# Optimization experiments

Measured on AMD Instinct MI355X. Metric: run time of the kernel, lower is better.

Reference implementation:

```python
import jax, jax.numpy as jnp
import numpy as np

N_NODES = 40000
N_EDGES = 640000
D = 128
N_LAYERS = 3


def setup_inputs() -> dict:
    key = jax.random.key(0)
    ks = jax.random.split(key, 6)
    x = jax.random.normal(ks[0], (N_NODES, D), dtype=jnp.float32)
    src = jax.random.randint(ks[1], (N_EDGES,), 0, N_NODES, dtype=jnp.int32)
    dst = jax.random.randint(ks[2], (N_EDGES,), 0, N_NODES, dtype=jnp.int32)
    scale = 1.0 / np.sqrt(D)
    w_self = jax.random.normal(ks[3], (N_LAYERS, D, D), dtype=jnp.float32) * scale
    w_neigh = jax.random.normal(ks[4], (N_LAYERS, D, D), dtype=jnp.float32) * scale
    b = jax.random.normal(ks[5], (N_LAYERS, D), dtype=jnp.float32) * scale
    return {"x": x, "src": src, "dst": dst, "w_self": w_self, "w_neigh": w_neigh, "b": b}


def reference(x, src, dst, w_self, w_neigh, b):
    # in-degree per destination node (clamped to avoid div-by-zero, matching mean aggregator)
    deg = jax.ops.segment_sum(jnp.ones_like(dst, dtype=x.dtype), dst, num_segments=N_NODES)
    inv_deg = (1.0 / jnp.maximum(deg, 1.0))[:, None]  # [N,1]

    h = x
    for l in range(N_LAYERS):
        # mean aggregation over in-neighbors: gather src feats, scatter-add to dst
        agg = jax.ops.segment_sum(h[src], dst, num_segments=N_NODES) * inv_deg  # [N,D]
        h = h @ w_self[l] + agg @ w_neigh[l] + b[l]  # SAGEConv: fc_self + fc_neigh + bias
        if l < N_LAYERS - 1:
            h = jax.nn.relu(h)  # dropout p=0.0 -> identity
    return h
```

## Files before the change

kernel.cpp:

```cpp
#include <hip/hip_runtime.h>

#define N_NODES 40000
#define N_EDGES 640000
#define DIM 128
#define N_LAYERS 3
#define STRIDE 64

typedef _Float16 half_t;
typedef __attribute__((ext_vector_type(8))) _Float16 f16x8_t;
typedef __attribute__((ext_vector_type(4))) float f32x4_t;

__global__ void scatterprep_kernel(const int* __restrict__ src, const int* __restrict__ dst,
                                   int* __restrict__ cnt, unsigned short* __restrict__ pcsr,
                                   const float* __restrict__ x, half_t* __restrict__ h,
                                   unsigned char* __restrict__ hq, float* __restrict__ hsc,
                                   const float* __restrict__ w_self, const float* __restrict__ w_neigh,
                                   half_t* __restrict__ wt) {
    const int SB = (N_EDGES + 255) / 256;
    if (blockIdx.x < SB) {
        int i = blockIdx.x * 256 + threadIdx.x;
        if (i < N_EDGES) {
            int d = dst[i];
            int pos = atomicAdd(&cnt[d], 1);
            if (pos < STRIDE) pcsr[d * STRIDE + pos] = (unsigned short)src[i];
        }
        return;
    }
    int i = (blockIdx.x - SB) * 256 + threadIdx.x;
    const int NS = N_NODES * DIM / 8;
    if (i < NS) {
        const float4* p = (const float4*)x + (size_t)i * 2;
        float4 a = p[0], b2 = p[1];
        float v[8] = {a.x, a.y, a.z, a.w, b2.x, b2.y, b2.z, b2.w};
        f16x8_t hv;
        float mx = 0.f;
#pragma unroll
        for (int j = 0; j < 8; ++j) {
            hv[j] = (half_t)v[j];
            mx = fmaxf(mx, fabsf((float)hv[j]));
        }
        *(f16x8_t*)&h[(size_t)i * 8] = hv;
        mx = fmaxf(mx, __shfl_xor(mx, 1));
        mx = fmaxf(mx, __shfl_xor(mx, 2));
        mx = fmaxf(mx, __shfl_xor(mx, 4));
        mx = fmaxf(mx, __shfl_xor(mx, 8));
        mx = fmaxf(mx, 1e-20f);
        float inv = 127.f / mx;
        unsigned int lo = 0, hi = 0;
#pragma unroll
        for (int j = 0; j < 4; ++j) {
            int q = (int)rintf((float)hv[j] * inv) + 128;
            lo |= ((unsigned int)q) << (8 * j);
        }
#pragma unroll
        for (int j = 0; j < 4; ++j) {
            int q = (int)rintf((float)hv[4 + j] * inv) + 128;
            hi |= ((unsigned int)q) << (8 * j);
        }
        uint2 pk; pk.x = lo; pk.y = hi;
        *(uint2*)&hq[(size_t)i * 8] = pk;
        if ((i & 15) == 0) hsc[i >> 4] = mx / 127.f;
    } else {
        int j = i - NS;
        if (j < N_LAYERS * 2 * DIM * DIM) {
            int k = j & (DIM - 1);
            int n = (j >> 7) & (DIM - 1);
            int ls = j >> 14;
            int l = ls >> 1, s = ls & 1;
            const float* W = (s ? w_neigh : w_self) + (size_t)l * DIM * DIM;
            wt[j] = (half_t)W[k * DIM + n];
        }
    }
}

__global__ void agg_kernel(const unsigned char* __restrict__ hq, const float* __restrict__ hsc,
                           const int* __restrict__ cnt, const unsigned short* __restrict__ pcsr,
                           half_t* __restrict__ agg) {
    int node = (blockIdx.x * blockDim.x + threadIdx.x) >> 6;
    int lane = threadIdx.x & 63;
    if (node >= N_NODES) return;
    const int g = lane >> 4, c = lane & 15;
    int deg = cnt[node];
    int nd = deg < STRIDE ? deg : STRIDE;
    int il = (lane < nd) ? (int)pcsr[node * STRIDE + lane] : 0;
    float sl = (lane < nd) ? hsc[il] : 0.f;

    float acc[8] = {0.f, 0.f, 0.f, 0.f, 0.f, 0.f, 0.f, 0.f};
    float ssum = 0.f;
    for (int base = 0; base < nd; base += 16) {
        float sf[4];
        int sidx[4];
        uint2 q[4];
#pragma unroll
        for (int s = 0; s < 4; ++s) {
            int ee = base + 4 * s + g;
            sidx[s] = __shfl(il, ee, 64);
            sf[s] = __shfl(sl, ee, 64);
            q[s] = *(const uint2*)&hq[(size_t)sidx[s] * DIM + c * 8];
        }
#pragma unroll
        for (int s = 0; s < 4; ++s) {
            ssum += sf[s];
            unsigned int lo = q[s].x, hi = q[s].y;
#pragma unroll
            for (int j = 0; j < 4; ++j)
                acc[j] = fmaf(sf[s], (float)((lo >> (8 * j)) & 0xFF), acc[j]);
#pragma unroll
            for (int j = 0; j < 4; ++j)
                acc[4 + j] = fmaf(sf[s], (float)((hi >> (8 * j)) & 0xFF), acc[4 + j]);
        }
    }
#pragma unroll
    for (int j = 0; j < 8; ++j) acc[j] -= 128.f * ssum;
#pragma unroll
    for (int j = 0; j < 8; ++j) {
        acc[j] += __shfl_xor(acc[j], 16, 64);
        acc[j] += __shfl_xor(acc[j], 32, 64);
    }
    if (g == 0) {
        float w = 1.0f / fmaxf((float)deg, 1.0f);
        f16x8_t o;
#pragma unroll
        for (int j = 0; j < 8; ++j) o[j] = (half_t)(acc[j] * w);
        *(f16x8_t*)&agg[(size_t)node * DIM + c * 8] = o;
    }
}

#define LDSN 136
#define SCRP 132
__global__ __launch_bounds__(256) void gemm_kernel(
    half_t* __restrict__ h, const half_t* __restrict__ agg,
    const half_t* __restrict__ wt,
    const float* __restrict__ bias, float* __restrict__ fout,
    unsigned char* __restrict__ hq, float* __restrict__ hsc,
    int write_f32, int relu) {
    __shared__ half_t sW[2 * DIM][LDSN];
    half_t (*sScr)[SCRP] = (half_t(*)[SCRP])sW;
    const int tid = threadIdx.x;
    const int wave = tid >> 6, lane = tid & 63;
    const int quad = lane >> 4, m = lane & 15;
    const int rowW = blockIdx.x * 128 + wave * 32;

#pragma unroll
    for (int c4 = 0; c4 < 16; ++c4) {
        int c = (c4 << 8) + tid;
        int part = c & 15;
        int n = c >> 4;
        *(f16x8_t*)&sW[n][part * 8] = *(const f16x8_t*)&wt[(size_t)n * DIM + part * 8];
    }
    __syncthreads();

    f32x4_t acc[2][8];
#pragma unroll
    for (int a = 0; a < 2; ++a)
#pragma unroll
        for (int b = 0; b < 8; ++b) acc[a][b] = {0.f, 0.f, 0.f, 0.f};

#pragma unroll
    for (int s = 0; s < 2; ++s) {
        const half_t* A = s ? agg : h;
        const int nb = s * DIM;
#pragma unroll
        for (int k2 = 0; k2 < 4; ++k2) {
            const int kg = (k2 << 5) + quad * 8;
            f16x8_t B[8];
#pragma unroll
            for (int jt = 0; jt < 8; ++jt)
                B[jt] = *(const f16x8_t*)&sW[nb + jt * 16 + m][kg];
#pragma unroll
            for (int rt = 0; rt < 2; ++rt) {
                int r = rowW + rt * 16 + m;
                r = (r < N_NODES) ? r : (N_NODES - 1);
                f16x8_t a = *(const f16x8_t*)&A[(size_t)r * DIM + kg];
#pragma unroll
                for (int jt = 0; jt < 8; ++jt)
                    acc[rt][jt] = __builtin_amdgcn_mfma_f32_16x16x32_f16(a, B[jt], acc[rt][jt], 0, 0, 0);
            }
        }
    }

    __syncthreads();

#pragma unroll
    for (int rt = 0; rt < 2; ++rt)
#pragma unroll
        for (int jt = 0; jt < 8; ++jt) {
            int col = jt * 16 + m;
            float bv = bias[col];
#pragma unroll
            for (int r4 = 0; r4 < 4; ++r4) {
                int rloc = wave * 32 + rt * 16 + quad * 4 + r4;
                int row = blockIdx.x * 128 + rloc;
                if (row >= N_NODES) continue;
                float v = acc[rt][jt][r4] + bv;
                if (relu) v = fmaxf(v, 0.f);
                if (write_f32) {
                    fout[(size_t)row * DIM + col] = v;
                } else {
                    half_t hv = (half_t)v;
                    h[(size_t)row * DIM + col] = hv;
                    sScr[rloc][col] = hv;
                }
            }
        }

    if (!write_f32) {
        __syncthreads();
        int rl = tid >> 1, hf = tid & 1;
        int row = blockIdx.x * 128 + rl;
        if (row < N_NODES) {
            float mx = 0.f;
#pragma unroll
            for (int k8 = 0; k8 < 8; ++k8) {
                f16x8_t vv = *(const f16x8_t*)&sScr[rl][hf * 64 + k8 * 8];
#pragma unroll
                for (int j = 0; j < 8; ++j) mx = fmaxf(mx, fabsf((float)vv[j]));
            }
            mx = fmaxf(mx, __shfl_xor(mx, 1));
            mx = fmaxf(mx, 1e-20f);
            float inv = 127.f / mx;
#pragma unroll
            for (int k8 = 0; k8 < 8; ++k8) {
                f16x8_t vv = *(const f16x8_t*)&sScr[rl][hf * 64 + k8 * 8];
                unsigned int lo = 0, hi = 0;
#pragma unroll
                for (int j = 0; j < 4; ++j)
                    lo |= ((unsigned int)((int)rintf((float)vv[j] * inv) + 128)) << (8 * j);
#pragma unroll
                for (int j = 0; j < 4; ++j)
                    hi |= ((unsigned int)((int)rintf((float)vv[4 + j] * inv) + 128)) << (8 * j);
                uint2 pk; pk.x = lo; pk.y = hi;
                *(uint2*)&hq[(size_t)row * DIM + hf * 64 + k8 * 8] = pk;
            }
            if (hf == 0) hsc[row] = mx / 127.f;
        }
    }
}


extern "C" void kernel_launch(void* const* d_in, const int* in_sizes, int n_in,
                              void* d_out, int out_size, void* d_ws, size_t ws_size,
                              hipStream_t stream) {
    const float* x      = (const float*)d_in[0];
    const int*   src    = (const int*)d_in[1];
    const int*   dst    = (const int*)d_in[2];
    const float* w_self = (const float*)d_in[3];
    const float* w_neigh= (const float*)d_in[4];
    const float* b      = (const float*)d_in[5];
    float* out = (float*)d_out;

    char* ws = (char*)d_ws;
    half_t* h    = (half_t*)ws;         ws += (size_t)N_NODES * DIM * 2;
    half_t* agg  = (half_t*)ws;         ws += (size_t)N_NODES * DIM * 2;
    half_t* wt   = (half_t*)ws;         ws += (size_t)N_LAYERS * 2 * DIM * DIM * 2;
    unsigned char* hq = (unsigned char*)ws; ws += (size_t)N_NODES * DIM;
    float* hsc   = (float*)ws;          ws += (size_t)N_NODES * 4;
    int*   cnt   = (int*)ws;            ws += (size_t)N_NODES * 4;
    unsigned short* pcsr = (unsigned short*)ws; ws += (size_t)N_NODES * STRIDE * 2;

    hipMemsetAsync(cnt, 0, (size_t)N_NODES * 4, stream);

    const int SB = (N_EDGES + 255) / 256;
    const int PREP_ITEMS = N_NODES * DIM / 8 + N_LAYERS * 2 * DIM * DIM;
    const int PB = (PREP_ITEMS + 255) / 256;
    scatterprep_kernel<<<SB + PB, 256, 0, stream>>>(src, dst, cnt, pcsr,
                                                    x, h, hq, hsc, w_self, w_neigh, wt);

    const int GEMM_BLOCKS = (N_NODES + 127) / 128;
    for (int l = 0; l < N_LAYERS; ++l) {
        agg_kernel<<<(N_NODES * 64 + 255) / 256, 256, 0, stream>>>(hq, hsc, cnt, pcsr, agg);
        int last = (l == N_LAYERS - 1);
        gemm_kernel<<<GEMM_BLOCKS, 256, 0, stream>>>(
            h, agg, wt + (size_t)l * 2 * DIM * DIM, b + (size_t)l * DIM,
            out, hq, hsc, last ? 1 : 0, last ? 0 : 1);
    }
}
```

Measured before the change: 227.6 us.

## Batch two edges per thread in scatter, widen CSR to int, grid-stride agg

The scatter phase now handles two edges per thread, issuing two atomics back to back to expose more memory-level parallelism with half as many blocks. The padded CSR neighbour list is widened from 16-bit to 32-bit indices, which doubles its footprint but avoids narrow stores. The aggregation kernel becomes a persistent grid-stride loop over nodes with a fixed grid of 2048 blocks instead of one wave per node. The fixed grid may balance load less evenly across CUs, and the larger CSR adds memory traffic.

```diff
diff --git a/kernel.cpp b/kernel.cpp
--- a/kernel.cpp
+++ b/kernel.cpp
@@ -11,18 +11,22 @@
 typedef __attribute__((ext_vector_type(4))) float f32x4_t;
 
 __global__ void scatterprep_kernel(const int* __restrict__ src, const int* __restrict__ dst,
-                                   int* __restrict__ cnt, unsigned short* __restrict__ pcsr,
+                                   int* __restrict__ cnt, int* __restrict__ pcsr,
                                    const float* __restrict__ x, half_t* __restrict__ h,
                                    unsigned char* __restrict__ hq, float* __restrict__ hsc,
                                    const float* __restrict__ w_self, const float* __restrict__ w_neigh,
                                    half_t* __restrict__ wt) {
-    const int SB = (N_EDGES + 255) / 256;
+    const int HALF = N_EDGES / 2;
+    const int SB = (HALF + 255) / 256;
     if (blockIdx.x < SB) {
         int i = blockIdx.x * 256 + threadIdx.x;
-        if (i < N_EDGES) {
-            int d = dst[i];
-            int pos = atomicAdd(&cnt[d], 1);
-            if (pos < STRIDE) pcsr[d * STRIDE + pos] = (unsigned short)src[i];
+        if (i < HALF) {
+            int d0 = dst[i], d1 = dst[i + HALF];
+            int s0 = src[i], s1 = src[i + HALF];
+            int p0 = atomicAdd(&cnt[d0], 1);
+            int p1 = atomicAdd(&cnt[d1], 1);
+            if (p0 < STRIDE) pcsr[d0 * STRIDE + p0] = s0;
+            if (p1 < STRIDE) pcsr[d1 * STRIDE + p1] = s1;
         }
         return;
     }
@@ -74,55 +78,58 @@
 }
 
 __global__ void agg_kernel(const unsigned char* __restrict__ hq, const float* __restrict__ hsc,
-                           const int* __restrict__ cnt, const unsigned short* __restrict__ pcsr,
+                           const int* __restrict__ cnt, const int* __restrict__ pcsr,
                            half_t* __restrict__ agg) {
-    int node = (blockIdx.x * blockDim.x + threadIdx.x) >> 6;
-    int lane = threadIdx.x & 63;
-    if (node >= N_NODES) return;
+    const int gw = (blockIdx.x * blockDim.x + threadIdx.x) >> 6;
+    const int nw = (gridDim.x * blockDim.x) >> 6;
+    const int lane = threadIdx.x & 63;
     const int g = lane >> 4, c = lane & 15;
-    int deg = cnt[node];
-    int nd = deg < STRIDE ? deg : STRIDE;
-    int il = (lane < nd) ? (int)pcsr[node * STRIDE + lane] : 0;
-    float sl = (lane < nd) ? hsc[il] : 0.f;
-
-    float acc[8] = {0.f, 0.f, 0.f, 0.f, 0.f, 0.f, 0.f, 0.f};
-    float ssum = 0.f;
-    for (int base = 0; base < nd; base += 16) {
-        float sf[4];
-        int sidx[4];
-        uint2 q[4];
-#pragma unroll
-        for (int s = 0; s < 4; ++s) {
-            int ee = base + 4 * s + g;
-            sidx[s] = __shfl(il, ee, 64);
-            sf[s] = __shfl(sl, ee, 64);
-            q[s] = *(const uint2*)&hq[(size_t)sidx[s] * DIM + c * 8];
-        }
-#pragma unroll
-        for (int s = 0; s < 4; ++s) {
-            ssum += sf[s];
-            unsigned int lo = q[s].x, hi = q[s].y;
-#pragma unroll
-            for (int j = 0; j < 4; ++j)
-                acc[j] = fmaf(sf[s], (float)((lo >> (8 * j)) & 0xFF), acc[j]);
-#pragma unroll
-            for (int j = 0; j < 4; ++j)
-                acc[4 + j] = fmaf(sf[s], (float)((hi >> (8 * j)) & 0xFF), acc[4 + j]);
-        }
-    }
-#pragma unroll
-    for (int j = 0; j < 8; ++j) acc[j] -= 128.f * ssum;
-#pragma unroll
-    for (int j = 0; j < 8; ++j) {
-        acc[j] += __shfl_xor(acc[j], 16, 64);
-        acc[j] += __shfl_xor(acc[j], 32, 64);
-    }
-    if (g == 0) {
-        float w = 1.0f / fmaxf((float)deg, 1.0f);
-        f16x8_t o;
-#pragma unroll
-        for (int j = 0; j < 8; ++j) o[j] = (half_t)(acc[j] * w);
-        *(f16x8_t*)&agg[(size_t)node * DIM + c * 8] = o;
+
+    for (int node = gw; node < N_NODES; node += nw) {
+        int deg = cnt[node];
+        int nd = deg < STRIDE ? deg : STRIDE;
+        int il = (lane < nd) ? pcsr[node * STRIDE + lane] : 0;
+        float sl = (lane < nd) ? hsc[il] : 0.f;
+
+        float acc[8] = {0.f, 0.f, 0.f, 0.f, 0.f, 0.f, 0.f, 0.f};
+        float ssum = 0.f;
+        for (int base = 0; base < nd; base += 16) {
+            float sf[4];
+            int sidx[4];
+            uint2 q[4];
+#pragma unroll
+            for (int s = 0; s < 4; ++s) {
+                int ee = base + 4 * s + g;
+                sidx[s] = __shfl(il, ee, 64);
+                sf[s] = __shfl(sl, ee, 64);
+                q[s] = *(const uint2*)&hq[(size_t)sidx[s] * DIM + c * 8];
+            }
+#pragma unroll
+            for (int s = 0; s < 4; ++s) {
+                ssum += sf[s];
+                unsigned int lo = q[s].x, hi = q[s].y;
+#pragma unroll
+                for (int j = 0; j < 4; ++j)
+                    acc[j] = fmaf(sf[s], (float)((lo >> (8 * j)) & 0xFF), acc[j]);
+#pragma unroll
+                for (int j = 0; j < 4; ++j)
+                    acc[4 + j] = fmaf(sf[s], (float)((hi >> (8 * j)) & 0xFF), acc[4 + j]);
+            }
+        }
+#pragma unroll
+        for (int j = 0; j < 8; ++j) acc[j] -= 128.f * ssum;
+#pragma unroll
+        for (int j = 0; j < 8; ++j) {
+            acc[j] += __shfl_xor(acc[j], 16, 64);
+            acc[j] += __shfl_xor(acc[j], 32, 64);
+        }
+        if (g == 0) {
+            float w = 1.0f / fmaxf((float)deg, 1.0f);
+            f16x8_t o;
+#pragma unroll
+            for (int j = 0; j < 8; ++j) o[j] = (half_t)(acc[j] * w);
+            *(f16x8_t*)&agg[(size_t)node * DIM + c * 8] = o;
+        }
     }
 }
 
@@ -256,11 +263,11 @@
     unsigned char* hq = (unsigned char*)ws; ws += (size_t)N_NODES * DIM;
     float* hsc   = (float*)ws;          ws += (size_t)N_NODES * 4;
     int*   cnt   = (int*)ws;            ws += (size_t)N_NODES * 4;
-    unsigned short* pcsr = (unsigned short*)ws; ws += (size_t)N_NODES * STRIDE * 2;
+    int*   pcsr  = (int*)ws;            ws += (size_t)N_NODES * STRIDE * 4;
 
     hipMemsetAsync(cnt, 0, (size_t)N_NODES * 4, stream);
 
-    const int SB = (N_EDGES + 255) / 256;
+    const int SB = (N_EDGES / 2 + 255) / 256;
     const int PREP_ITEMS = N_NODES * DIM / 8 + N_LAYERS * 2 * DIM * DIM;
     const int PB = (PREP_ITEMS + 255) / 256;
     scatterprep_kernel<<<SB + PB, 256, 0, stream>>>(src, dst, cnt, pcsr,
@@ -268,7 +275,7 @@
 
     const int GEMM_BLOCKS = (N_NODES + 127) / 128;
     for (int l = 0; l < N_LAYERS; ++l) {
-        agg_kernel<<<(N_NODES * 64 + 255) / 256, 256, 0, stream>>>(hq, hsc, cnt, pcsr, agg);
+        agg_kernel<<<2048, 256, 0, stream>>>(hq, hsc, cnt, pcsr, agg);
         int last = (l == N_LAYERS - 1);
         gemm_kernel<<<GEMM_BLOCKS, 256, 0, stream>>>(
             h, agg, wt + (size_t)l * 2 * DIM * DIM, b + (size_t)l * DIM,
```

New measurement: 226.8 us. About the same (-0.3%).
